# Performance work log

Measured on AMD Instinct MI355X. Metric: run time of the kernel, lower is better.

The kernel has to match this reference:

```python
import jax, jax.numpy as jnp
import numpy as np

L, H, P = 8192, 512, 512


def setup_inputs() -> dict:
    key = jax.random.key(0)
    ks = jax.random.split(key, 7)
    u = jax.random.normal(ks[0], (L, H), dtype=jnp.float32)
    # diagonal continuous-time state matrix Lambda = Lambda_re + i*Lambda_im (stable: Re < 0)
    Lambda_re = -0.5 * jax.random.uniform(ks[1], (P,), dtype=jnp.float32) - 0.1
    Lambda_im = jnp.pi * jax.random.normal(ks[2], (P,), dtype=jnp.float32)
    # B_tilde (P,H) and C_tilde (H,P) parameterized as real/imag pairs (..., 2)
    B = jax.random.normal(ks[3], (P, H, 2), dtype=jnp.float32) / np.sqrt(2.0 * H)
    C = jax.random.normal(ks[4], (H, P, 2), dtype=jnp.float32) / np.sqrt(2.0 * P)
    D = jax.random.normal(ks[5], (H,), dtype=jnp.float32)
    log_step = jax.random.uniform(ks[6], (P,), dtype=jnp.float32,
                                  minval=np.log(1e-3), maxval=np.log(1e-1))
    return {"u": u, "Lambda_re": Lambda_re, "Lambda_im": Lambda_im,
            "B": B, "C": C, "D": D, "log_step": log_step}


def _binop(qi, qj):
    # binary operator for parallel scan of diagonal linear recurrence
    A_i, Bu_i = qi
    A_j, Bu_j = qj
    return (A_j * A_i, A_j * Bu_i + Bu_j)


def reference(u, Lambda_re, Lambda_im, B, C, D, log_step):
    Lambda = (Lambda_re + 1j * Lambda_im).astype(jnp.complex64)          # (P,)
    B_tilde = (B[..., 0] + 1j * B[..., 1]).astype(jnp.complex64)         # (P,H)
    C_tilde = (C[..., 0] + 1j * C[..., 1]).astype(jnp.complex64)         # (H,P)
    Delta = jnp.exp(log_step)                                            # (P,)
    # zero-order-hold discretization
    Lambda_bar = jnp.exp(Lambda * Delta)                                 # (P,)
    B_bar = ((Lambda_bar - 1.0) / Lambda)[:, None] * B_tilde             # (P,H)
    # Bu_t = B_bar @ u_t for all t  -> (L,P)
    Bu = jnp.einsum('lh,ph->lp', u.astype(jnp.complex64), B_bar)
    A_elems = jnp.broadcast_to(Lambda_bar, (u.shape[0], P))              # (L,P)
    _, xs = jax.lax.associative_scan(_binop, (A_elems, Bu), axis=0)      # (L,P) states
    # y_t = Re(C_tilde @ x_t) + D * u_t
    y = jnp.einsum('lp,hp->lh', xs, C_tilde).real + D * u
    return y
```

## Files before the change

kernel.cpp:

```cpp
#include <hip/hip_runtime.h>
#include <hip/hip_bf16.h>

#define L_DIM 8192
#define H_DIM 512
#define P_DIM 512
#define CHUNK 32
#define NCHUNK (L_DIM / CHUNK)

typedef __attribute__((ext_vector_type(8))) short bf16x8;
typedef __attribute__((ext_vector_type(4))) float f32x4;

__device__ inline short f2bf(float x) {
    union { float f; unsigned u; } v; v.f = x;
    unsigned r = v.u + 0x7fffu + ((v.u >> 16) & 1u);
    return (short)(r >> 16);
}
__device__ inline float bflo2f(unsigned w) {
    union { unsigned u; float f; } v; v.u = w << 16; return v.f;
}
__device__ inline float bfhi2f(unsigned w) {
    union { unsigned u; float f; } v; v.u = w & 0xffff0000u; return v.f;
}

__device__ inline void gload_lds16(const void* g, void* l) {
    __builtin_amdgcn_global_load_lds(
        (const __attribute__((address_space(1))) unsigned int*)g,
        (__attribute__((address_space(3))) unsigned int*)l, 16, 0, 0);
}

template<int N> __device__ inline void waitcnt_vm() {
    if constexpr (N == 0)      asm volatile("s_waitcnt vmcnt(0)" ::: "memory");
    else if constexpr (N == 3) asm volatile("s_waitcnt vmcnt(3)" ::: "memory");
    else if constexpr (N == 4) asm volatile("s_waitcnt vmcnt(4)" ::: "memory");
    else if constexpr (N == 6) asm volatile("s_waitcnt vmcnt(6)" ::: "memory");
    else if constexpr (N == 8) asm volatile("s_waitcnt vmcnt(8)" ::: "memory");
}

__global__ __launch_bounds__(256) void k_prep(
        const float* __restrict__ Lre, const float* __restrict__ Lim,
        const float* __restrict__ Bin, const float* __restrict__ log_step,
        const float* __restrict__ Cin, const float* __restrict__ u,
        short* __restrict__ Bcat, short* __restrict__ Ccat,
        short* __restrict__ u_bf,
        float* __restrict__ lambda_bar, float* __restrict__ lambda_powN) {
    const int blk = blockIdx.x;
    const int tid = threadIdx.x;
    if (blk < P_DIM) {
        int p = blk;
        float lr = Lre[p], li = Lim[p];
        float dt = expf(log_step[p]);
        float ar = lr * dt, ai = li * dt;
        float er = expf(ar);
        float lbr = er * cosf(ai);
        float lbi = er * sinf(ai);
        float nr = lbr - 1.0f, ni = lbi;
        float den = lr * lr + li * li;
        float fr = (nr * lr + ni * li) / den;
        float fi = (ni * lr - nr * li) / den;
        if (tid == 0) {
            lambda_bar[2 * p] = lbr;
            lambda_bar[2 * p + 1] = lbi;
            float eN = expf(ar * (float)CHUNK);
            lambda_powN[2 * p] = eN * cosf(ai * (float)CHUNK);
            lambda_powN[2 * p + 1] = eN * sinf(ai * (float)CHUNK);
        }
        for (int h = tid; h < H_DIM; h += 256) {
            float br = Bin[((size_t)p * H_DIM + h) * 2 + 0];
            float bi = Bin[((size_t)p * H_DIM + h) * 2 + 1];
            Bcat[(size_t)(2 * p) * H_DIM + h] = f2bf(fr * br - fi * bi);
            Bcat[(size_t)(2 * p + 1) * H_DIM + h] = f2bf(fr * bi + fi * br);
        }
    } else if (blk < P_DIM + 1024) {
        int idx = (blk - P_DIM) * 256 + tid;
        int h = idx >> 9, p = idx & 511;
        float cr = Cin[(size_t)idx * 2 + 0];
        float ci = Cin[(size_t)idx * 2 + 1];
        Ccat[(size_t)h * (2 * P_DIM) + 2 * p + 0] = f2bf(cr);
        Ccat[(size_t)h * (2 * P_DIM) + 2 * p + 1] = f2bf(-ci);
    } else {
        int i = (blk - P_DIM - 1024) * 256 + tid;
        const float4* uf = (const float4*)u;
        float4 a0 = uf[(size_t)i * 2];
        float4 a1 = uf[(size_t)i * 2 + 1];
        bf16x8 sv;
        sv[0] = f2bf(a0.x); sv[1] = f2bf(a0.y); sv[2] = f2bf(a0.z); sv[3] = f2bf(a0.w);
        sv[4] = f2bf(a1.x); sv[5] = f2bf(a1.y); sv[6] = f2bf(a1.z); sv[7] = f2bf(a1.w);
        *(bf16x8*)&u_bf[(size_t)i * 8] = sv;
    }
}

template<int BN, bool OBF16, bool EPI>
__global__ __launch_bounds__(256) void k_gemm(
        const short* __restrict__ A, const short* __restrict__ B,
        void* __restrict__ Cout, int M, int N, int K, int nwgn,
        const float* __restrict__ Dv, const short* __restrict__ Ubf) {
    constexpr int NF = BN / 32;
    constexpr int LPS = 2 + BN / 64;
    __shared__ short As[3][128 * 32];
    __shared__ short Bs[3][BN * 32];

    const int tid = threadIdx.x;
    const int lane = tid & 63;
    const int wid = tid >> 6;
    const int wr = wid >> 1, wc = wid & 1;

    const int nwg = gridDim.x;
    const int orig = blockIdx.x;
    const int id = (orig & 7) * (nwg >> 3) + (orig >> 3);
    const int bm = (id / nwgn) * 128;
    const int bn = (id % nwgn) * BN;

    f32x4 acc[4][NF] = {};
    const int arow = wr * 64 + (lane & 15);
    const int brow = wc * (BN / 2) + (lane & 15);
    const int rslot = (((lane >> 4) ^ (lane & 3) ^ ((lane >> 2) & 3)) << 4);

    auto stage = [&](int buf, int kk) {
#pragma unroll
        for (int q = 0; q < 2; ++q) {
            int sb = q * 4096 + tid * 16;
            int row = sb >> 6, slot = (sb >> 4) & 3;
            int gs = slot ^ ((row ^ (row >> 2)) & 3);
            const char* src = (const char*)A + ((size_t)(bm + row) * K + kk) * 2 + gs * 16;
            gload_lds16(src, (char*)&As[buf][0] + sb);
        }
#pragma unroll
        for (int q = 0; q < BN / 64; ++q) {
            int sb = q * 4096 + tid * 16;
            int row = sb >> 6, slot = (sb >> 4) & 3;
            int gs = slot ^ ((row ^ (row >> 2)) & 3);
            const char* src = (const char*)B + ((size_t)(bn + row) * K + kk) * 2 + gs * 16;
            gload_lds16(src, (char*)&Bs[buf][0] + sb);
        }
    };

    const int nt = K >> 5;
    stage(0, 0);
    stage(1, 32);

    int cur = 0, stg = 2;
    for (int t = 0; t < nt; ++t) {
        if (t + 2 < nt) {
            stage(stg, (t + 2) * 32);
            waitcnt_vm<2 * LPS>();
        } else if (t + 1 < nt) {
            waitcnt_vm<LPS>();
        } else {
            waitcnt_vm<0>();
        }
        __builtin_amdgcn_s_barrier();
        __builtin_amdgcn_sched_barrier(0);

        const char* Ab = (const char*)&As[cur][0];
        const char* Bb = (const char*)&Bs[cur][0];
        bf16x8 af[4], bfr[NF];
#pragma unroll
        for (int m = 0; m < 4; ++m)
            af[m] = *(const bf16x8*)(Ab + (arow + m * 16) * 64 + rslot);
#pragma unroll
        for (int n = 0; n < NF; ++n)
            bfr[n] = *(const bf16x8*)(Bb + (brow + n * 16) * 64 + rslot);
#pragma unroll
        for (int m = 0; m < 4; ++m)
#pragma unroll
            for (int n = 0; n < NF; ++n)
                acc[m][n] = __builtin_amdgcn_mfma_f32_16x16x32_bf16(af[m], bfr[n], acc[m][n], 0, 0, 0);

        if (t + 1 < nt) __builtin_amdgcn_s_barrier();
        cur = (cur == 2) ? 0 : cur + 1;
        stg = (stg == 2) ? 0 : stg + 1;
    }

    const int fq = lane >> 4, fr = lane & 15;
#pragma unroll
    for (int m = 0; m < 4; ++m) {
#pragma unroll
        for (int n = 0; n < NF; ++n) {
            int col = bn + wc * (BN / 2) + n * 16 + fr;
            int row0 = bm + wr * 64 + m * 16 + fq * 4;
#pragma unroll
            for (int j = 0; j < 4; ++j) {
                int row = row0 + j;
                float v = acc[m][n][j];
                if (OBF16) {
                    ((short*)Cout)[(size_t)row * N + col] = f2bf(v);
                } else {
                    if (EPI) {
                        union { unsigned u; float f; } ub;
                        ub.u = ((unsigned)(unsigned short)Ubf[(size_t)row * N + col]) << 16;
                        v += Dv[col] * ub.f;
                    }
                    ((float*)Cout)[(size_t)row * N + col] = v;
                }
            }
        }
    }
}

__global__ __launch_bounds__(256) void k_scan_summary(const unsigned* __restrict__ Bu,
                                                      const float* __restrict__ lambda_bar,
                                                      float* __restrict__ S) {
    int gid = blockIdx.x * blockDim.x + threadIdx.x;
    int c = gid >> 9, p = gid & 511;
    float lr = lambda_bar[2 * p], li = lambda_bar[2 * p + 1];
    float xr = 0.f, xi = 0.f;
    const unsigned* bu = Bu + (size_t)c * CHUNK * P_DIM + p;
#pragma unroll 4
    for (int j = 0; j < CHUNK; ++j) {
        unsigned w = bu[(size_t)j * P_DIM];
        float br = bflo2f(w), bi = bfhi2f(w);
        float nxr = lr * xr - li * xi + br;
        float nxi = lr * xi + li * xr + bi;
        xr = nxr; xi = nxi;
    }
    ((float2*)S)[(size_t)c * P_DIM + p] = make_float2(xr, xi);
}

__global__ __launch_bounds__(512) void k_scan_apply(const unsigned* __restrict__ Bu,
                                                    unsigned* __restrict__ XsB,
                                                    const float* __restrict__ lambda_bar,
                                                    const float* __restrict__ lambda_powN,
                                                    const float* __restrict__ S) {
    const int c = blockIdx.x;
    const int p = threadIdx.x;
    const float lNr = lambda_powN[2 * p], lNi = lambda_powN[2 * p + 1];
    float xr = 0.f, xi = 0.f;
    const float2* Sp = (const float2*)S;
    int d = 0;
    while (d + 8 <= c) {
        float2 sb[8];
#pragma unroll
        for (int j = 0; j < 8; ++j) sb[j] = Sp[(size_t)(d + j) * P_DIM + p];
#pragma unroll
        for (int j = 0; j < 8; ++j) {
            float nxr = lNr * xr - lNi * xi + sb[j].x;
            float nxi = lNr * xi + lNi * xr + sb[j].y;
            xr = nxr; xi = nxi;
        }
        d += 8;
    }
    for (; d < c; ++d) {
        float2 s = Sp[(size_t)d * P_DIM + p];
        float nxr = lNr * xr - lNi * xi + s.x;
        float nxi = lNr * xi + lNi * xr + s.y;
        xr = nxr; xi = nxi;
    }
    const float lr = lambda_bar[2 * p], li = lambda_bar[2 * p + 1];
    const unsigned* bu = Bu + (size_t)c * CHUNK * P_DIM + p;
#pragma unroll 4
    for (int j = 0; j < CHUNK; ++j) {
        unsigned w = bu[(size_t)j * P_DIM];
        float br = bflo2f(w), bi = bfhi2f(w);
        float nxr = lr * xr - li * xi + br;
        float nxi = lr * xi + li * xr + bi;
        xr = nxr; xi = nxi;
        unsigned pk = (unsigned)(unsigned short)f2bf(xr)
                    | ((unsigned)(unsigned short)f2bf(xi) << 16);
        XsB[((size_t)c * CHUNK + j) * P_DIM + p] = pk;
    }
}

extern "C" void kernel_launch(void* const* d_in, const int* in_sizes, int n_in,
                              void* d_out, int out_size, void* d_ws, size_t ws_size,
                              hipStream_t stream) {
    const float* u        = (const float*)d_in[0];
    const float* Lre      = (const float*)d_in[1];
    const float* Lim      = (const float*)d_in[2];
    const float* Bin      = (const float*)d_in[3];
    const float* Cin      = (const float*)d_in[4];
    const float* Dv       = (const float*)d_in[5];
    const float* log_step = (const float*)d_in[6];
    float* y = (float*)d_out;

    char* w = (char*)d_ws;
    size_t off = 0;
    short* Bcat = (short*)(w + off); off += (size_t)2 * P_DIM * H_DIM * 2;
    short* Ccat = (short*)(w + off); off += (size_t)2 * P_DIM * H_DIM * 2;
    float* lamb = (float*)(w + off); off += 2 * P_DIM * 4;
    float* lamN = (float*)(w + off); off += 2 * P_DIM * 4;
    float* S    = (float*)(w + off); off += (size_t)NCHUNK * 2 * P_DIM * 4;
    unsigned* Bu  = (unsigned*)(w + off); off += (size_t)L_DIM * P_DIM * 4;
    unsigned* XsB = (unsigned*)(w + off); off += (size_t)L_DIM * P_DIM * 4;
    short* u_bf   = (short*)(w + off);   off += (size_t)L_DIM * H_DIM * 2;

    k_prep<<<P_DIM + 1024 + 2048, 256, 0, stream>>>(
        Lre, Lim, Bin, log_step, Cin, u, Bcat, Ccat, u_bf, lamb, lamN);
    k_gemm<128, true, false><<<(L_DIM / 128) * ((2 * P_DIM) / 128), 256, 0, stream>>>(
        u_bf, Bcat, (void*)Bu, L_DIM, 2 * P_DIM, H_DIM, (2 * P_DIM) / 128,
        nullptr, nullptr);
    k_scan_summary<<<(NCHUNK * P_DIM) / 256, 256, 0, stream>>>(Bu, lamb, S);
    k_scan_apply<<<NCHUNK, 512, 0, stream>>>(Bu, XsB, lamb, lamN, S);
    k_gemm<64, false, true><<<(L_DIM / 128) * (H_DIM / 64), 256, 0, stream>>>(
        (const short*)XsB, Ccat, (void*)y, L_DIM, H_DIM, 2 * P_DIM, H_DIM / 64,
        Dv, u_bf);
}
```

Baseline: 78.91 us.

## Fuse chunk scan summaries into Bu GEMM epilogue and restructure scan into three phases

```diff
diff --git a/kernel.cpp b/kernel.cpp
--- a/kernel.cpp
+++ b/kernel.cpp
@@ -89,15 +89,17 @@
     }
 }
 
-template<int BN, bool OBF16, bool EPI>
+template<int BN, bool OBF16, bool EPI, bool SUMM>
 __global__ __launch_bounds__(256) void k_gemm(
         const short* __restrict__ A, const short* __restrict__ B,
         void* __restrict__ Cout, int M, int N, int K, int nwgn,
-        const float* __restrict__ Dv, const short* __restrict__ Ubf) {
+        const float* __restrict__ Dv, const short* __restrict__ Ubf,
+        const float* __restrict__ Lamb, float* __restrict__ S) {
     constexpr int NF = BN / 32;
     constexpr int LPS = 2 + BN / 64;
-    __shared__ short As[3][128 * 32];
-    __shared__ short Bs[3][BN * 32];
+    constexpr int ASZ = 128 * 32 * 2;
+    constexpr int BSZ = BN * 32 * 2;
+    __shared__ char smem[3 * ASZ + 3 * BSZ];
 
     const int tid = threadIdx.x;
     const int lane = tid & 63;
@@ -122,7 +124,7 @@
             int row = sb >> 6, slot = (sb >> 4) & 3;
             int gs = slot ^ ((row ^ (row >> 2)) & 3);
             const char* src = (const char*)A + ((size_t)(bm + row) * K + kk) * 2 + gs * 16;
-            gload_lds16(src, (char*)&As[buf][0] + sb);
+            gload_lds16(src, smem + buf * ASZ + sb);
         }
 #pragma unroll
         for (int q = 0; q < BN / 64; ++q) {
@@ -130,7 +132,7 @@
             int row = sb >> 6, slot = (sb >> 4) & 3;
             int gs = slot ^ ((row ^ (row >> 2)) & 3);
             const char* src = (const char*)B + ((size_t)(bn + row) * K + kk) * 2 + gs * 16;
-            gload_lds16(src, (char*)&Bs[buf][0] + sb);
+            gload_lds16(src, smem + 3 * ASZ + buf * BSZ + sb);
         }
     };
 
@@ -151,8 +153,8 @@
         __builtin_amdgcn_s_barrier();
         __builtin_amdgcn_sched_barrier(0);
 
-        const char* Ab = (const char*)&As[cur][0];
-        const char* Bb = (const char*)&Bs[cur][0];
+        const char* Ab = smem + cur * ASZ;
+        const char* Bb = smem + 3 * ASZ + cur * BSZ;
         bf16x8 af[4], bfr[NF];
 #pragma unroll
         for (int m = 0; m < 4; ++m)
@@ -160,16 +162,20 @@
 #pragma unroll
         for (int n = 0; n < NF; ++n)
             bfr[n] = *(const bf16x8*)(Bb + (brow + n * 16) * 64 + rslot);
+        __builtin_amdgcn_s_setprio(1);
 #pragma unroll
         for (int m = 0; m < 4; ++m)
 #pragma unroll
             for (int n = 0; n < NF; ++n)
                 acc[m][n] = __builtin_amdgcn_mfma_f32_16x16x32_bf16(af[m], bfr[n], acc[m][n], 0, 0, 0);
+        __builtin_amdgcn_s_setprio(0);
 
         if (t + 1 < nt) __builtin_amdgcn_s_barrier();
         cur = (cur == 2) ? 0 : cur + 1;
         stg = (stg == 2) ? 0 : stg + 1;
     }
+
+    if (SUMM) __syncthreads();
 
     const int fq = lane >> 4, fr = lane & 15;
 #pragma unroll
@@ -183,7 +189,13 @@
                 int row = row0 + j;
                 float v = acc[m][n][j];
                 if (OBF16) {
-                    ((short*)Cout)[(size_t)row * N + col] = f2bf(v);
+                    short s = f2bf(v);
+                    ((short*)Cout)[(size_t)row * N + col] = s;
+                    if (SUMM) {
+                        int rowL = (wr * 64 + m * 16 + fq * 4 + j);
+                        int colL = (wc * (BN / 2) + n * 16 + fr);
+                        *(short*)(smem + rowL * 264 + colL * 2) = s;
+                    }
                 } else {
                     if (EPI) {
                         union { unsigned u; float f; } ub;
@@ -195,57 +207,58 @@
             }
         }
     }
-}
-
-__global__ __launch_bounds__(256) void k_scan_summary(const unsigned* __restrict__ Bu,
-                                                      const float* __restrict__ lambda_bar,
-                                                      float* __restrict__ S) {
-    int gid = blockIdx.x * blockDim.x + threadIdx.x;
-    int c = gid >> 9, p = gid & 511;
-    float lr = lambda_bar[2 * p], li = lambda_bar[2 * p + 1];
-    float xr = 0.f, xi = 0.f;
-    const unsigned* bu = Bu + (size_t)c * CHUNK * P_DIM + p;
-#pragma unroll 4
-    for (int j = 0; j < CHUNK; ++j) {
-        unsigned w = bu[(size_t)j * P_DIM];
-        float br = bflo2f(w), bi = bfhi2f(w);
-        float nxr = lr * xr - li * xi + br;
-        float nxi = lr * xi + li * xr + bi;
-        xr = nxr; xi = nxi;
-    }
-    ((float2*)S)[(size_t)c * P_DIM + p] = make_float2(xr, xi);
-}
-
-__global__ __launch_bounds__(512) void k_scan_apply(const unsigned* __restrict__ Bu,
-                                                    unsigned* __restrict__ XsB,
-                                                    const float* __restrict__ lambda_bar,
-                                                    const float* __restrict__ lambda_powN,
-                                                    const float* __restrict__ S) {
-    const int c = blockIdx.x;
-    const int p = threadIdx.x;
-    const float lNr = lambda_powN[2 * p], lNi = lambda_powN[2 * p + 1];
+
+    if (SUMM) {
+        __syncthreads();
+        const int c_loc = tid >> 6;
+        const int ch = tid & 63;
+        const int gch = (bn >> 1) + ch;
+        const float lr = Lamb[2 * gch], li = Lamb[2 * gch + 1];
+        float xr = 0.f, xi = 0.f;
+#pragma unroll 8
+        for (int j = 0; j < 32; ++j) {
+            int rowL = c_loc * 32 + j;
+            unsigned wv = *(const unsigned*)(smem + rowL * 264 + ch * 4);
+            float br = bflo2f(wv), bi = bfhi2f(wv);
+            float nxr = lr * xr - li * xi + br;
+            float nxi = lr * xi + li * xr + bi;
+            xr = nxr; xi = nxi;
+        }
+        ((float2*)S)[(size_t)((bm >> 5) + c_loc) * P_DIM + gch] = make_float2(xr, xi);
+    }
+}
+
+__global__ __launch_bounds__(64) void k_scan_combine(const float* __restrict__ S,
+                                                     const float* __restrict__ lambda_powN,
+                                                     float* __restrict__ pref) {
+    const int ch = blockIdx.x * 64 + threadIdx.x;
+    const float lNr = lambda_powN[2 * ch], lNi = lambda_powN[2 * ch + 1];
     float xr = 0.f, xi = 0.f;
     const float2* Sp = (const float2*)S;
-    int d = 0;
-    while (d + 8 <= c) {
-        float2 sb[8];
-#pragma unroll
-        for (int j = 0; j < 8; ++j) sb[j] = Sp[(size_t)(d + j) * P_DIM + p];
-#pragma unroll
-        for (int j = 0; j < 8; ++j) {
+    float2* Pp = (float2*)pref;
+    for (int c0 = 0; c0 < NCHUNK; c0 += 16) {
+        float2 sb[16];
+#pragma unroll
+        for (int j = 0; j < 16; ++j) sb[j] = Sp[(size_t)(c0 + j) * P_DIM + ch];
+#pragma unroll
+        for (int j = 0; j < 16; ++j) {
+            Pp[(size_t)(c0 + j) * P_DIM + ch] = make_float2(xr, xi);
             float nxr = lNr * xr - lNi * xi + sb[j].x;
             float nxi = lNr * xi + lNi * xr + sb[j].y;
             xr = nxr; xi = nxi;
         }
-        d += 8;
-    }
-    for (; d < c; ++d) {
-        float2 s = Sp[(size_t)d * P_DIM + p];
-        float nxr = lNr * xr - lNi * xi + s.x;
-        float nxi = lNr * xi + lNi * xr + s.y;
-        xr = nxr; xi = nxi;
-    }
+    }
+}
+
+__global__ __launch_bounds__(256) void k_scan_apply(const unsigned* __restrict__ Bu,
+                                                    unsigned* __restrict__ XsB,
+                                                    const float* __restrict__ lambda_bar,
+                                                    const float* __restrict__ pref) {
+    int gid = blockIdx.x * blockDim.x + threadIdx.x;
+    int c = gid >> 9, p = gid & 511;
     const float lr = lambda_bar[2 * p], li = lambda_bar[2 * p + 1];
+    float2 x0 = ((const float2*)pref)[(size_t)c * P_DIM + p];
+    float xr = x0.x, xi = x0.y;
     const unsigned* bu = Bu + (size_t)c * CHUNK * P_DIM + p;
 #pragma unroll 4
     for (int j = 0; j < CHUNK; ++j) {
@@ -279,18 +292,19 @@
     float* lamb = (float*)(w + off); off += 2 * P_DIM * 4;
     float* lamN = (float*)(w + off); off += 2 * P_DIM * 4;
     float* S    = (float*)(w + off); off += (size_t)NCHUNK * 2 * P_DIM * 4;
+    float* pref = (float*)(w + off); off += (size_t)NCHUNK * 2 * P_DIM * 4;
     unsigned* Bu  = (unsigned*)(w + off); off += (size_t)L_DIM * P_DIM * 4;
     unsigned* XsB = (unsigned*)(w + off); off += (size_t)L_DIM * P_DIM * 4;
     short* u_bf   = (short*)(w + off);   off += (size_t)L_DIM * H_DIM * 2;
 
     k_prep<<<P_DIM + 1024 + 2048, 256, 0, stream>>>(
         Lre, Lim, Bin, log_step, Cin, u, Bcat, Ccat, u_bf, lamb, lamN);
-    k_gemm<128, true, false><<<(L_DIM / 128) * ((2 * P_DIM) / 128), 256, 0, stream>>>(
+    k_gemm<128, true, false, true><<<(L_DIM / 128) * ((2 * P_DIM) / 128), 256, 0, stream>>>(
         u_bf, Bcat, (void*)Bu, L_DIM, 2 * P_DIM, H_DIM, (2 * P_DIM) / 128,
-        nullptr, nullptr);
-    k_scan_summary<<<(NCHUNK * P_DIM) / 256, 256, 0, stream>>>(Bu, lamb, S);
-    k_scan_apply<<<NCHUNK, 512, 0, stream>>>(Bu, XsB, lamb, lamN, S);
-    k_gemm<64, false, true><<<(L_DIM / 128) * (H_DIM / 64), 256, 0, stream>>>(
+        nullptr, nullptr, lamb, S);
+    k_scan_combine<<<8, 64, 0, stream>>>(S, lamN, pref);
+    k_scan_apply<<<(NCHUNK * P_DIM) / 256, 256, 0, stream>>>(Bu, XsB, lamb, pref);
+    k_gemm<64, false, true, false><<<(L_DIM / 128) * (H_DIM / 64), 256, 0, stream>>>(
         (const short*)XsB, Ccat, (void*)y, L_DIM, H_DIM, 2 * P_DIM, H_DIM / 64,
-        Dv, u_bf);
-}
+        Dv, u_bf, nullptr, nullptr);
+}
```

Result: faster. 69.69 us (-11.7%).
